# Optimization experiments

Hardware: AMD Instinct MI355X
Metric: run time of the kernel (lower is better)

## Reference

```python
import jax, jax.numpy as jnp
import numpy as np

THRESHOLD = 0.5
DILATION_ITERS = 5  # scipy binary_dilation(iterations=5)


def _dilate_cross(mask, iters=DILATION_ITERS):
    # mask: [T, H, W] bool. scipy's default 3D structure on a [H,W,1] frame
    # degenerates to a 2D 4-connected (cross) structuring element.
    # One iteration = OR of center and the 4 axis-aligned neighbors.
    for _ in range(iters):
        p = jnp.pad(mask, ((0, 0), (1, 1), (1, 1)))
        mask = (p[:, 1:-1, 1:-1]
                | p[:, :-2, 1:-1] | p[:, 2:, 1:-1]
                | p[:, 1:-1, :-2] | p[:, 1:-1, 2:])
    return mask


def setup_inputs() -> dict:
    key = jax.random.key(0)
    k1, k2 = jax.random.split(key)
    X = jax.random.normal(k1, (3, 128, 256, 256), dtype=jnp.float32)          # [C,T,H,W]
    background = jax.random.normal(k2, (256, 256, 3), dtype=jnp.float32)      # [H,W,C]
    return {"X": X, "background": background}


def reference(X, background):
    Xp = jnp.transpose(X, (1, 2, 3, 0))                                       # [T,H,W,C]
    mask = jnp.sum(jnp.abs(Xp - background), axis=-1) > THRESHOLD             # [T,H,W]
    mask = _dilate_cross(mask)
    out = Xp * mask[..., None].astype(Xp.dtype)
    return jnp.transpose(out, (3, 0, 1, 2))                                   # [C,T,H,W]
```

## Files before the change

kernel.cpp:

```cpp
#include <hip/hip_runtime.h>
#include <stdint.h>

#define TT 128
#define HH 256
#define WW 256
#define PLANE (TT*HH*WW)
#define FRAME (HH*WW)
#define ROWS 32
#define HALO 5
#define BROWS (ROWS + 2*HALO)
#define THRESH 0.5f

typedef float nfloat4 __attribute__((ext_vector_type(4)));

__device__ __forceinline__ uint64_t shfl64(uint64_t v, int src) {
    uint32_t lo = (uint32_t)v, hi = (uint32_t)(v >> 32);
    lo = __shfl(lo, src);
    hi = __shfl(hi, src);
    return ((uint64_t)hi << 32) | lo;
}

__device__ __forceinline__ uint64_t pack16(uint32_t nib) {
    int lane = threadIdx.x & 63;
    uint64_t v = (uint64_t)nib << (4 * (lane & 15));
    v |= __shfl_xor(v, 1);
    v |= __shfl_xor(v, 2);
    v |= __shfl_xor(v, 4);
    v |= __shfl_xor(v, 8);
    return v;
}

__device__ __forceinline__ uint32_t mask_nib(const float* __restrict__ X,
                                             const float* __restrict__ bg,
                                             int t, int gr, int col4) {
    if (gr < 0 || gr >= HH) return 0u;
    size_t pix = (size_t)t * FRAME + (size_t)gr * WW + 4 * col4;
    nfloat4 x0 = *(const nfloat4*)(X + pix);
    nfloat4 x1 = *(const nfloat4*)(X + (size_t)PLANE + pix);
    nfloat4 x2 = *(const nfloat4*)(X + 2 * (size_t)PLANE + pix);
    const nfloat4* bp = (const nfloat4*)(bg + ((size_t)gr * WW + 4 * col4) * 3);
    nfloat4 q0 = bp[0], q1 = bp[1], q2 = bp[2];
    uint32_t nib = 0;
    nib |= ((fabsf(x0[0] - q0[0]) + fabsf(x1[0] - q0[1]) + fabsf(x2[0] - q0[2])) > THRESH) ? 1u : 0u;
    nib |= ((fabsf(x0[1] - q0[3]) + fabsf(x1[1] - q1[0]) + fabsf(x2[1] - q1[1])) > THRESH) ? 2u : 0u;
    nib |= ((fabsf(x0[2] - q1[2]) + fabsf(x1[2] - q1[3]) + fabsf(x2[2] - q2[0])) > THRESH) ? 4u : 0u;
    nib |= ((fabsf(x0[3] - q2[1]) + fabsf(x1[3] - q2[2]) + fabsf(x2[3] - q2[3])) > THRESH) ? 8u : 0u;
    return nib;
}

__global__ __launch_bounds__(512) void fused_kernel(const float* __restrict__ X,
                                                    const float* __restrict__ bg,
                                                    float* __restrict__ out) {
    __shared__ uint64_t buf[BROWS][4];
    const int t    = blockIdx.x >> 3;
    const int j    = blockIdx.x & 7;
    const int r0   = j * ROWS;
    const int tid  = threadIdx.x;
    const int lane = tid & 63;
    const int wave = tid >> 6;
    const int col4 = lane;

    nfloat4 xv[4][3];
#pragma unroll
    for (int k = 0; k < 4; ++k) {
        const int row = wave + 8 * k;
        const int gr  = r0 + row;
        size_t pix = (size_t)t * FRAME + (size_t)gr * WW + 4 * col4;
        xv[k][0] = *(const nfloat4*)(X + pix);
        xv[k][1] = *(const nfloat4*)(X + (size_t)PLANE + pix);
        xv[k][2] = *(const nfloat4*)(X + 2 * (size_t)PLANE + pix);
        asm volatile("" : "+v"(xv[k][0]), "+v"(xv[k][1]), "+v"(xv[k][2]));
        const nfloat4* bp = (const nfloat4*)(bg + ((size_t)gr * WW + 4 * col4) * 3);
        nfloat4 q0 = bp[0], q1 = bp[1], q2 = bp[2];
        uint32_t nib = 0;
        nib |= ((fabsf(xv[k][0][0] - q0[0]) + fabsf(xv[k][1][0] - q0[1]) + fabsf(xv[k][2][0] - q0[2])) > THRESH) ? 1u : 0u;
        nib |= ((fabsf(xv[k][0][1] - q0[3]) + fabsf(xv[k][1][1] - q1[0]) + fabsf(xv[k][2][1] - q1[1])) > THRESH) ? 2u : 0u;
        nib |= ((fabsf(xv[k][0][2] - q1[2]) + fabsf(xv[k][1][2] - q1[3]) + fabsf(xv[k][2][2] - q2[0])) > THRESH) ? 4u : 0u;
        nib |= ((fabsf(xv[k][0][3] - q2[1]) + fabsf(xv[k][1][3] - q2[2]) + fabsf(xv[k][2][3] - q2[3])) > THRESH) ? 8u : 0u;
        uint64_t w = pack16(nib);
        if ((lane & 15) == 0) buf[HALO + row][lane >> 4] = w;
    }

    {
        const int slot = wave;
        const int gr   = (slot < 5) ? (r0 - HALO + slot) : (r0 + ROWS + (slot - 5));
        const int brow = (slot < 5) ? slot : (HALO + ROWS + (slot - 5));
        uint64_t w = pack16(mask_nib(X, bg, t, gr, col4));
        if ((lane & 15) == 0) buf[brow][lane >> 4] = w;
    }
    if (tid < 128) {
        const int slot = 8 + wave;
        const int gr   = r0 + ROWS + (slot - 5);
        const int brow = HALO + ROWS + (slot - 5);
        uint64_t w = pack16(mask_nib(X, bg, t, gr, col4));
        if ((lane & 15) == 0) buf[brow][lane >> 4] = w;
    }
    __syncthreads();

    if (wave == 0) {
        uint64_t r_[4];
#pragma unroll
        for (int i = 0; i < 4; ++i) r_[i] = (lane < BROWS) ? buf[lane][i] : 0ULL;
#pragma unroll
        for (int it = 0; it < 5; ++it) {
            uint64_t nr[4];
#pragma unroll
            for (int i = 0; i < 4; ++i) {
                uint64_t c = r_[i];
                uint64_t l = (i > 0) ? r_[i - 1] : 0ULL;
                uint64_t rr = (i < 3) ? r_[i + 1] : 0ULL;
                uint64_t u = shfl64(c, lane - 1);
                uint64_t d = shfl64(c, lane + 1);
                u = (lane == 0) ? 0ULL : u;
                nr[i] = c | (c << 1) | (l >> 63) | (c >> 1) | (rr << 63) | u | d;
            }
#pragma unroll
            for (int i = 0; i < 4; ++i) r_[i] = nr[i];
        }
        if (lane >= HALO && lane < HALO + ROWS) {
#pragma unroll
            for (int i = 0; i < 4; ++i) buf[lane][i] = r_[i];
        }
    }
    __syncthreads();

#pragma unroll
    for (int k = 0; k < 4; ++k) {
        const int row = wave + 8 * k;
        const int gr  = r0 + row;
        uint64_t w = buf[HALO + row][col4 >> 4];
        uint32_t nb = (uint32_t)(w >> (4 * (col4 & 15))) & 0xFu;
        float m0 = (float)(nb & 1u);
        float m1 = (float)((nb >> 1) & 1u);
        float m2 = (float)((nb >> 2) & 1u);
        float m3 = (float)((nb >> 3) & 1u);
        size_t pix = (size_t)t * FRAME + (size_t)gr * WW + 4 * col4;
#pragma unroll
        for (int c = 0; c < 3; ++c) {
            nfloat4 v = xv[k][c];
            nfloat4 nv = { v[0] * m0, v[1] * m1, v[2] * m2, v[3] * m3 };
            __builtin_nontemporal_store(nv, (nfloat4*)(out + (size_t)c * PLANE + pix));
        }
    }
}

extern "C" void kernel_launch(void* const* d_in, const int* in_sizes, int n_in,
                              void* d_out, int out_size, void* d_ws, size_t ws_size,
                              hipStream_t stream) {
    const float* X  = (const float*)d_in[0];
    const float* bg = (const float*)d_in[1];
    float* out = (float*)d_out;
    const int nblocks = TT * (HH / ROWS);
    fused_kernel<<<nblocks, 512, 0, stream>>>(X, bg, out);
}
```

Before: 41.92 us.

## Loop each block over four row tiles with redundant per-wave dilation

Each block now handles four consecutive 32-row tiles of a frame instead of one, so the grid shrinks from 1024 to 256 blocks of 512 threads. Every wave runs the bitmask dilation redundantly from shared memory and gets its rows' masks by shuffles, which removes the second barrier and the write-back to shared memory. The mask buffer is double-buffered across tile iterations, so only one __syncthreads is needed per tile. In exchange there are fewer blocks in flight to hide memory latency (256 blocks on a device with many CUs), and the shuffle work is repeated in all eight waves.

```diff
diff --git a/kernel.cpp b/kernel.cpp
--- a/kernel.cpp
+++ b/kernel.cpp
@@ -7,6 +7,8 @@
 #define PLANE (TT*HH*WW)
 #define FRAME (HH*WW)
 #define ROWS 32
+#define TPF  (HH/ROWS)
+#define REPEAT 4
 #define HALO 5
 #define BROWS (ROWS + 2*HALO)
 #define THRESH 0.5f
@@ -51,95 +53,102 @@
 __global__ __launch_bounds__(512) void fused_kernel(const float* __restrict__ X,
                                                     const float* __restrict__ bg,
                                                     float* __restrict__ out) {
-    __shared__ uint64_t buf[BROWS][4];
-    const int t    = blockIdx.x >> 3;
-    const int j    = blockIdx.x & 7;
-    const int r0   = j * ROWS;
+    __shared__ uint64_t mbuf[2][BROWS][4];
+    const int t    = blockIdx.x >> 1;
+    const int j0   = (blockIdx.x & 1) * REPEAT;
     const int tid  = threadIdx.x;
     const int lane = tid & 63;
     const int wave = tid >> 6;
     const int col4 = lane;
 
-    nfloat4 xv[4][3];
 #pragma unroll
-    for (int k = 0; k < 4; ++k) {
-        const int row = wave + 8 * k;
-        const int gr  = r0 + row;
-        size_t pix = (size_t)t * FRAME + (size_t)gr * WW + 4 * col4;
-        xv[k][0] = *(const nfloat4*)(X + pix);
-        xv[k][1] = *(const nfloat4*)(X + (size_t)PLANE + pix);
-        xv[k][2] = *(const nfloat4*)(X + 2 * (size_t)PLANE + pix);
-        asm volatile("" : "+v"(xv[k][0]), "+v"(xv[k][1]), "+v"(xv[k][2]));
-        const nfloat4* bp = (const nfloat4*)(bg + ((size_t)gr * WW + 4 * col4) * 3);
-        nfloat4 q0 = bp[0], q1 = bp[1], q2 = bp[2];
-        uint32_t nib = 0;
-        nib |= ((fabsf(xv[k][0][0] - q0[0]) + fabsf(xv[k][1][0] - q0[1]) + fabsf(xv[k][2][0] - q0[2])) > THRESH) ? 1u : 0u;
-        nib |= ((fabsf(xv[k][0][1] - q0[3]) + fabsf(xv[k][1][1] - q1[0]) + fabsf(xv[k][2][1] - q1[1])) > THRESH) ? 2u : 0u;
-        nib |= ((fabsf(xv[k][0][2] - q1[2]) + fabsf(xv[k][1][2] - q1[3]) + fabsf(xv[k][2][2] - q2[0])) > THRESH) ? 4u : 0u;
-        nib |= ((fabsf(xv[k][0][3] - q2[1]) + fabsf(xv[k][1][3] - q2[2]) + fabsf(xv[k][2][3] - q2[3])) > THRESH) ? 8u : 0u;
-        uint64_t w = pack16(nib);
-        if ((lane & 15) == 0) buf[HALO + row][lane >> 4] = w;
-    }
+    for (int rep = 0; rep < REPEAT; ++rep) {
+        const int r0 = (j0 + rep) * ROWS;
+        uint64_t (*B)[4] = mbuf[rep & 1];
 
-    {
-        const int slot = wave;
-        const int gr   = (slot < 5) ? (r0 - HALO + slot) : (r0 + ROWS + (slot - 5));
-        const int brow = (slot < 5) ? slot : (HALO + ROWS + (slot - 5));
-        uint64_t w = pack16(mask_nib(X, bg, t, gr, col4));
-        if ((lane & 15) == 0) buf[brow][lane >> 4] = w;
-    }
-    if (tid < 128) {
-        const int slot = 8 + wave;
-        const int gr   = r0 + ROWS + (slot - 5);
-        const int brow = HALO + ROWS + (slot - 5);
-        uint64_t w = pack16(mask_nib(X, bg, t, gr, col4));
-        if ((lane & 15) == 0) buf[brow][lane >> 4] = w;
-    }
-    __syncthreads();
+        nfloat4 xv[4][3];
+        uint32_t nib[4];
+#pragma unroll
+        for (int k = 0; k < 4; ++k) {
+            const int gr = r0 + wave + 8 * k;
+            size_t pix = (size_t)t * FRAME + (size_t)gr * WW + 4 * col4;
+            xv[k][0] = *(const nfloat4*)(X + pix);
+            xv[k][1] = *(const nfloat4*)(X + (size_t)PLANE + pix);
+            xv[k][2] = *(const nfloat4*)(X + 2 * (size_t)PLANE + pix);
+            const nfloat4* bp = (const nfloat4*)(bg + ((size_t)gr * WW + 4 * col4) * 3);
+            nfloat4 q0 = bp[0], q1 = bp[1], q2 = bp[2];
+            uint32_t nb = 0;
+            nb |= ((fabsf(xv[k][0][0] - q0[0]) + fabsf(xv[k][1][0] - q0[1]) + fabsf(xv[k][2][0] - q0[2])) > THRESH) ? 1u : 0u;
+            nb |= ((fabsf(xv[k][0][1] - q0[3]) + fabsf(xv[k][1][1] - q1[0]) + fabsf(xv[k][2][1] - q1[1])) > THRESH) ? 2u : 0u;
+            nb |= ((fabsf(xv[k][0][2] - q1[2]) + fabsf(xv[k][1][2] - q1[3]) + fabsf(xv[k][2][2] - q2[0])) > THRESH) ? 4u : 0u;
+            nb |= ((fabsf(xv[k][0][3] - q2[1]) + fabsf(xv[k][1][3] - q2[2]) + fabsf(xv[k][2][3] - q2[3])) > THRESH) ? 8u : 0u;
+            nib[k] = nb;
+        }
+#pragma unroll
+        for (int k = 0; k < 4; ++k) {
+            uint64_t w = pack16(nib[k]);
+            if ((lane & 15) == 0) B[HALO + wave + 8 * k][lane >> 4] = w;
+        }
+        {
+            const int slot = wave;
+            const int gr   = (slot < 5) ? (r0 - HALO + slot) : (r0 + ROWS + (slot - 5));
+            const int brow = (slot < 5) ? slot : (HALO + ROWS + (slot - 5));
+            uint64_t w = pack16(mask_nib(X, bg, t, gr, col4));
+            if ((lane & 15) == 0) B[brow][lane >> 4] = w;
+        }
+        if (tid < 128) {
+            const int slot = 8 + wave;
+            const int gr   = r0 + ROWS + (slot - 5);
+            const int brow = HALO + ROWS + (slot - 5);
+            uint64_t w = pack16(mask_nib(X, bg, t, gr, col4));
+            if ((lane & 15) == 0) B[brow][lane >> 4] = w;
+        }
+        __syncthreads();
 
-    if (wave == 0) {
         uint64_t r_[4];
 #pragma unroll
-        for (int i = 0; i < 4; ++i) r_[i] = (lane < BROWS) ? buf[lane][i] : 0ULL;
+        for (int i = 0; i < 4; ++i) r_[i] = (lane < BROWS) ? B[lane][i] : 0ULL;
 #pragma unroll
         for (int it = 0; it < 5; ++it) {
             uint64_t nr[4];
 #pragma unroll
             for (int i = 0; i < 4; ++i) {
-                uint64_t c = r_[i];
-                uint64_t l = (i > 0) ? r_[i - 1] : 0ULL;
+                uint64_t c  = r_[i];
+                uint64_t l  = (i > 0) ? r_[i - 1] : 0ULL;
                 uint64_t rr = (i < 3) ? r_[i + 1] : 0ULL;
-                uint64_t u = shfl64(c, lane - 1);
-                uint64_t d = shfl64(c, lane + 1);
+                uint64_t u  = shfl64(c, lane - 1);
+                uint64_t d  = shfl64(c, lane + 1);
                 u = (lane == 0) ? 0ULL : u;
                 nr[i] = c | (c << 1) | (l >> 63) | (c >> 1) | (rr << 63) | u | d;
             }
 #pragma unroll
             for (int i = 0; i < 4; ++i) r_[i] = nr[i];
         }
-        if (lane >= HALO && lane < HALO + ROWS) {
-#pragma unroll
-            for (int i = 0; i < 4; ++i) buf[lane][i] = r_[i];
-        }
-    }
-    __syncthreads();
 
 #pragma unroll
-    for (int k = 0; k < 4; ++k) {
-        const int row = wave + 8 * k;
-        const int gr  = r0 + row;
-        uint64_t w = buf[HALO + row][col4 >> 4];
-        uint32_t nb = (uint32_t)(w >> (4 * (col4 & 15))) & 0xFu;
-        float m0 = (float)(nb & 1u);
-        float m1 = (float)((nb >> 1) & 1u);
-        float m2 = (float)((nb >> 2) & 1u);
-        float m3 = (float)((nb >> 3) & 1u);
-        size_t pix = (size_t)t * FRAME + (size_t)gr * WW + 4 * col4;
+        for (int k = 0; k < 4; ++k) {
+            const int row = wave + 8 * k;
+            const int src = HALO + row;
+            uint64_t t0 = shfl64(r_[0], src);
+            uint64_t t1 = shfl64(r_[1], src);
+            uint64_t t2 = shfl64(r_[2], src);
+            uint64_t t3 = shfl64(r_[3], src);
+            const int idx = lane >> 4;
+            uint64_t lo = (idx & 1) ? t1 : t0;
+            uint64_t hi = (idx & 1) ? t3 : t2;
+            uint64_t w  = (idx & 2) ? hi : lo;
+            uint32_t nb = (uint32_t)(w >> (4 * (lane & 15))) & 0xFu;
+            float m0 = (float)(nb & 1u);
+            float m1 = (float)((nb >> 1) & 1u);
+            float m2 = (float)((nb >> 2) & 1u);
+            float m3 = (float)((nb >> 3) & 1u);
+            size_t pix = (size_t)t * FRAME + (size_t)(r0 + row) * WW + 4 * col4;
 #pragma unroll
-        for (int c = 0; c < 3; ++c) {
-            nfloat4 v = xv[k][c];
-            nfloat4 nv = { v[0] * m0, v[1] * m1, v[2] * m2, v[3] * m3 };
-            __builtin_nontemporal_store(nv, (nfloat4*)(out + (size_t)c * PLANE + pix));
+            for (int c = 0; c < 3; ++c) {
+                nfloat4 v = xv[k][c];
+                nfloat4 nv = { v[0] * m0, v[1] * m1, v[2] * m2, v[3] * m3 };
+                __builtin_nontemporal_store(nv, (nfloat4*)(out + (size_t)c * PLANE + pix));
+            }
         }
     }
 }
@@ -150,6 +159,6 @@
     const float* X  = (const float*)d_in[0];
     const float* bg = (const float*)d_in[1];
     float* out = (float*)d_out;
-    const int nblocks = TT * (HH / ROWS);
+    const int nblocks = TT * (TPF / REPEAT);
     fused_kernel<<<nblocks, 512, 0, stream>>>(X, bg, out);
 }
```

Result: slower. 44.16 us (+5.3%).
